# Kernel tuning notes

Hardware: AMD Instinct MI355X
Metric: run time of the kernel (lower is better)

The kernel has to match this reference:

```python
import jax, jax.numpy as jnp
import numpy as np
import math

B, S, D = 2, 2048, 1024
H, KV, HD = 16, 4, 64
N_REP = H // KV
ROPE_THETA = 1.0e6


def _rope_tables(seq_len, head_dim, theta):
    inv_freq = 1.0 / (theta ** (np.arange(0, head_dim, 2, dtype=np.float32) / head_dim))
    t = np.arange(seq_len, dtype=np.float32)
    freqs = np.outer(t, inv_freq)                      # [S, HD/2]
    emb = np.concatenate([freqs, freqs], axis=-1)      # [S, HD]
    return jnp.asarray(np.cos(emb)), jnp.asarray(np.sin(emb))


def setup_inputs() -> dict:
    key = jax.random.key(0)
    ks = jax.random.split(key, 6)
    cos, sin = _rope_tables(S, HD, ROPE_THETA)
    scale = 0.02
    return {
        "x": jax.random.normal(ks[0], (B, S, D), dtype=jnp.float32),
        "cos": cos,
        "sin": sin,
        "Wq": jax.random.normal(ks[1], (D, H * HD), dtype=jnp.float32) * scale,
        "Wk": jax.random.normal(ks[2], (D, KV * HD), dtype=jnp.float32) * scale,
        "Wv": jax.random.normal(ks[3], (D, KV * HD), dtype=jnp.float32) * scale,
        "Wo": jax.random.normal(ks[4], (H * HD, D), dtype=jnp.float32) * scale,
    }


def _rotate_half(u):
    u1, u2 = u[..., : HD // 2], u[..., HD // 2 :]
    return jnp.concatenate([-u2, u1], axis=-1)


def reference(x, cos, sin, Wq, Wk, Wv, Wo):
    bsz, seq_len, _ = x.shape
    q = (x @ Wq).reshape(bsz, seq_len, H, HD)   # [B,S,H,HD]
    k = (x @ Wk).reshape(bsz, seq_len, KV, HD)  # [B,S,KV,HD]
    v = (x @ Wv).reshape(bsz, seq_len, KV, HD)

    # RoPE: cos/sin [S,HD] broadcast over batch and heads (unsqueeze_dim=1)
    c = cos[:seq_len][None, :, None, :]
    s = sin[:seq_len][None, :, None, :]
    q = q * c + _rotate_half(q) * s
    k = k * c + _rotate_half(k) * s

    # repeat_kv: expand KV heads groupwise to H heads
    k = jnp.repeat(k, N_REP, axis=2)  # [B,S,H,HD]
    v = jnp.repeat(v, N_REP, axis=2)

    q = q.transpose(0, 2, 1, 3)  # [B,H,S,HD]
    k = k.transpose(0, 2, 1, 3)
    v = v.transpose(0, 2, 1, 3)

    scores = jnp.einsum("bhqd,bhkd->bhqk", q, k) / math.sqrt(HD)
    causal = jnp.tril(jnp.ones((seq_len, seq_len), dtype=bool))
    scores = jnp.where(causal[None, None], scores, jnp.finfo(jnp.float32).min)
    probs = jax.nn.softmax(scores.astype(jnp.float32), axis=-1).astype(x.dtype)

    out = jnp.einsum("bhqk,bhkd->bhqd", probs, v)        # [B,H,S,HD]
    out = out.transpose(0, 2, 1, 3).reshape(bsz, seq_len, H * HD)
    return out @ Wo
```

## Files before the change

### kernel.cpp

```cpp
#include <hip/hip_runtime.h>

#define SS 2048
#define NH 16
#define NKV 4
#define HD 64

typedef __bf16 bf16;
typedef __bf16 bf16x4 __attribute__((ext_vector_type(4)));
typedef __bf16 bf16x8 __attribute__((ext_vector_type(8)));
typedef float f32x4 __attribute__((ext_vector_type(4)));

#define SM_SCALE 0.18033688011f

__device__ __forceinline__ void gl_lds16(const bf16* g, bf16* l) {
    __builtin_amdgcn_global_load_lds((const __attribute__((address_space(1))) void*)g,
                                     (__attribute__((address_space(3))) void*)l, 16, 0, 0);
}

__global__ __launch_bounds__(256) void prep_kernel(
    const float* __restrict__ x,
    const float* __restrict__ Wq, const float* __restrict__ Wk,
    const float* __restrict__ Wv, const float* __restrict__ Wo,
    bf16* __restrict__ wqkv_t, bf16* __restrict__ wo_t, bf16* __restrict__ xb)
{
    const int blk = blockIdx.x;
    const int tid = threadIdx.x;
    if (blk >= 640) {
        const size_t i0 = (size_t)(blk - 640) * 16384;
        #pragma unroll
        for (int i = 0; i < 16; ++i) {
            const size_t idx = i0 + i * 1024 + tid * 4;
            const float4 v = *(const float4*)&x[idx];
            bf16x4 o4;
            o4[0] = (bf16)v.x; o4[1] = (bf16)v.y; o4[2] = (bf16)v.z; o4[3] = (bf16)v.w;
            *(bf16x4*)&xb[idx] = o4;
        }
        return;
    }
    const float* W; bf16* Wt; int N, n0, k0;
    if (blk < 256)      { W = Wq; Wt = wqkv_t;                       N = 1024; n0 = (blk & 15) * 64;         k0 = (blk >> 4) * 64; }
    else if (blk < 320) { W = Wk; Wt = wqkv_t + (size_t)1024 * 1024; N = 256;  n0 = ((blk - 256) & 3) * 64;  k0 = ((blk - 256) >> 2) * 64; }
    else if (blk < 384) { W = Wv; Wt = wqkv_t + (size_t)1280 * 1024; N = 256;  n0 = ((blk - 320) & 3) * 64;  k0 = ((blk - 320) >> 2) * 64; }
    else                { W = Wo; Wt = wo_t;                         N = 1024; n0 = ((blk - 384) & 15) * 64; k0 = ((blk - 384) >> 4) * 64; }

    __shared__ float Ts[64][65];
    const int c = tid & 63, rr = tid >> 6;
    #pragma unroll
    for (int i = 0; i < 16; ++i) {
        const int kk = i * 4 + rr;
        Ts[kk][c] = W[(size_t)(k0 + kk) * N + n0 + c];
    }
    __syncthreads();
    #pragma unroll
    for (int i = 0; i < 16; ++i) {
        const int nn = i * 4 + rr;
        Wt[(size_t)(n0 + nn) * 1024 + k0 + c] = (bf16)Ts[c][nn];
    }
}

template<int EPI>
__global__ __launch_bounds__(256) void gemm_bt_kernel(
    const bf16* __restrict__ A, const bf16* __restrict__ Bt, float* __restrict__ C,
    const float* __restrict__ cosp, const float* __restrict__ sinp,
    bf16* __restrict__ qo, bf16* __restrict__ ko, bf16* __restrict__ vto,
    int N, int K, int CB)
{
    __shared__ bf16 As[2][64 * 64];
    __shared__ bf16 Bs[2][128 * 64];
    const int bid = blockIdx.x;
    const int j = bid >> 3;
    const int rb = (bid & 7) + 8 * (j / CB);
    const int cb = j % CB;
    const int m0 = rb * 64, n0 = cb * 128;
    const int tid = threadIdx.x;
    const int w = tid >> 6, lane = tid & 63, g = lane >> 4, li = lane & 15;
    const int wm = w >> 1, wn = w & 1;

    f32x4 acc[2][4];
    const f32x4 z = {0.f, 0.f, 0.f, 0.f};
    #pragma unroll
    for (int i = 0; i < 2; ++i)
        #pragma unroll
        for (int jj = 0; jj < 4; ++jj) acc[i][jj] = z;

    const int srow = tid >> 3;
    const int schunk = ((tid & 7) ^ (srow & 7)) * 8;
    const bf16* pA[2];
    const bf16* pB[4];
    #pragma unroll
    for (int s = 0; s < 2; ++s) pA[s] = A + (size_t)(m0 + s * 32 + srow) * K + schunk;
    #pragma unroll
    for (int s = 0; s < 4; ++s) pB[s] = Bt + (size_t)(n0 + s * 32 + srow) * K + schunk;
    const int lw = w * 512;

    const int NT = K >> 6;

    #pragma unroll
    for (int s = 0; s < 2; ++s) gl_lds16(pA[s], &As[0][s * 2048 + lw]);
    #pragma unroll
    for (int s = 0; s < 4; ++s) gl_lds16(pB[s], &Bs[0][s * 2048 + lw]);
    #pragma unroll
    for (int s = 0; s < 2; ++s) gl_lds16(pA[s] + 64, &As[1][s * 2048 + lw]);
    #pragma unroll
    for (int s = 0; s < 4; ++s) gl_lds16(pB[s] + 64, &Bs[1][s * 2048 + lw]);

    for (int t = 0; t < NT; ++t) {
        const int cur = t & 1;
        if (t + 1 < NT) { asm volatile("s_waitcnt vmcnt(6)" ::: "memory"); }
        else            { asm volatile("s_waitcnt vmcnt(0)" ::: "memory"); }
        __builtin_amdgcn_s_barrier();
        #pragma unroll
        for (int tt = 0; tt < 2; ++tt) {
            const int phys = ((tt * 4 + g) ^ (li & 7)) * 8;
            bf16x8 af[2], bfr[4];
            #pragma unroll
            for (int mi = 0; mi < 2; ++mi) af[mi] = *(const bf16x8*)&As[cur][(wm * 32 + mi * 16 + li) * 64 + phys];
            #pragma unroll
            for (int ni = 0; ni < 4; ++ni) bfr[ni] = *(const bf16x8*)&Bs[cur][(wn * 64 + ni * 16 + li) * 64 + phys];
            __builtin_amdgcn_s_setprio(1);
            #pragma unroll
            for (int mi = 0; mi < 2; ++mi)
                #pragma unroll
                for (int ni = 0; ni < 4; ++ni)
                    acc[mi][ni] = __builtin_amdgcn_mfma_f32_16x16x32_bf16(af[mi], bfr[ni], acc[mi][ni], 0, 0, 0);
            __builtin_amdgcn_s_setprio(0);
        }
        __builtin_amdgcn_s_barrier();
        if (t + 2 < NT) {
            const int kk = (t + 2) << 6;
            #pragma unroll
            for (int s = 0; s < 2; ++s) gl_lds16(pA[s] + kk, &As[cur][s * 2048 + lw]);
            #pragma unroll
            for (int s = 0; s < 4; ++s) gl_lds16(pB[s] + kk, &Bs[cur][s * 2048 + lw]);
        }
    }

    const int row0 = m0 + wm * 32, col0 = n0 + wn * 64;
    if (EPI == 0) {
        #pragma unroll
        for (int mi = 0; mi < 2; ++mi)
            #pragma unroll
            for (int ni = 0; ni < 4; ++ni)
                #pragma unroll
                for (int r = 0; r < 4; ++r)
                    C[(size_t)(row0 + mi * 16 + g * 4 + r) * N + col0 + ni * 16 + li] = acc[mi][ni][r];
    } else {
        #pragma unroll
        for (int ni = 0; ni < 4; ++ni) {
            const int col = col0 + ni * 16 + li;
            const int d = col & 63;
            #pragma unroll
            for (int mi = 0; mi < 2; ++mi) {
                #pragma unroll
                for (int r = 0; r < 4; ++r) {
                    const int row = row0 + mi * 16 + g * 4 + r;
                    const int bb = row >> 11, s = row & 2047;
                    float val = acc[mi][ni][r];
                    if (col < 1280) {
                        const float pairv = acc[mi][ni ^ 2][r];
                        const float rot = (d < 32) ? -pairv : pairv;
                        val = val * cosp[s * 64 + d] + rot * sinp[s * 64 + d];
                    }
                    if (col < 1024) {
                        const int hh = col >> 6;
                        qo[(((size_t)bb * NH + hh) * SS + s) * HD + d] = (bf16)(val * SM_SCALE);
                    } else if (col < 1280) {
                        const int kh = (col - 1024) >> 6;
                        ko[(((size_t)bb * NKV + kh) * SS + s) * HD + d] = (bf16)val;
                    } else {
                        const int kh = (col - 1280) >> 6;
                        vto[(((size_t)bb * NKV + kh) * HD + d) * SS + s] = (bf16)val;
                    }
                }
            }
        }
    }
}

__global__ __launch_bounds__(256) void flash_kernel(const bf16* __restrict__ q, const bf16* __restrict__ k,
                                                    const bf16* __restrict__ vt, bf16* __restrict__ o)
{
    __shared__ bf16 Ks[2][64 * 64];
    __shared__ bf16 Vt[2][64 * 64];
    __shared__ bf16 Ps[4][16 * 64];

    const int blk = blockIdx.x;
    const int qt = 31 - (blk >> 5);
    const int h = blk & 15;
    const int b = (blk >> 4) & 1;
    const int kvh = h >> 2;
    const int tid = threadIdx.x;
    const int w = tid >> 6, lane = tid & 63, g = lane >> 4, li = lane & 15;

    const bf16* qh = q + ((size_t)b * NH + h) * SS * HD;
    const bf16* kh = k + ((size_t)b * NKV + kvh) * SS * HD;
    const bf16* vh = vt + ((size_t)b * NKV + kvh) * (size_t)HD * SS;

    bf16x8 ones;
    #pragma unroll
    for (int jj = 0; jj < 8; ++jj) ones[jj] = (bf16)1.0f;
    const f32x4 z = {0.f, 0.f, 0.f, 0.f};

    const bf16* qrow = qh + (size_t)(qt * 64 + w * 16 + li) * HD;
    bf16x8 qf[2];
    qf[0] = *(const bf16x8*)(qrow + g * 8);
    qf[1] = *(const bf16x8*)(qrow + 32 + g * 8);

    const int srow = tid >> 3;
    const int schunk = ((tid & 7) ^ (srow & 7)) * 8;
    const int lw = w * 512;

    const int xm = (li & 7) << 1;

    f32x4 o_acc[4], l_acc;
    #pragma unroll
    for (int nt = 0; nt < 4; ++nt) o_acc[nt] = z;
    l_acc = z;

    #pragma unroll
    for (int s = 0; s < 2; ++s)
        gl_lds16(kh + (size_t)(s * 32 + srow) * HD + schunk, &Ks[0][s * 2048 + lw]);
    #pragma unroll
    for (int s = 0; s < 2; ++s)
        gl_lds16(vh + (size_t)(s * 32 + srow) * SS + schunk, &Vt[0][s * 2048 + lw]);
    if (qt >= 1) {
        #pragma unroll
        for (int s = 0; s < 2; ++s)
            gl_lds16(kh + (size_t)(64 + s * 32 + srow) * HD + schunk, &Ks[1][s * 2048 + lw]);
        #pragma unroll
        for (int s = 0; s < 2; ++s)
            gl_lds16(vh + (size_t)(s * 32 + srow) * SS + 64 + schunk, &Vt[1][s * 2048 + lw]);
    }

    for (int kt = 0; kt <= qt; ++kt) {
        const int cur = kt & 1;
        if (kt < qt) { asm volatile("s_waitcnt vmcnt(4)" ::: "memory"); }
        else         { asm volatile("s_waitcnt vmcnt(0)" ::: "memory"); }
        __builtin_amdgcn_s_barrier();

        f32x4 s_acc[4];
        #pragma unroll
        for (int nt = 0; nt < 4; ++nt) s_acc[nt] = z;
        __builtin_amdgcn_s_setprio(1);
        #pragma unroll
        for (int t = 0; t < 2; ++t)
            #pragma unroll
            for (int nt = 0; nt < 4; ++nt) {
                const bf16x8 kf = *(const bf16x8*)&Ks[cur][(nt * 16 + li) * 64 + (((t * 4 + g) ^ (li & 7)) * 8)];
                s_acc[nt] = __builtin_amdgcn_mfma_f32_16x16x32_bf16(kf, qf[t], s_acc[nt], 0, 0, 0);
            }
        __builtin_amdgcn_s_setprio(0);

        if (kt == qt) {
            const int qrow_in = w * 16 + li;
            #pragma unroll
            for (int nt = 0; nt < 4; ++nt) {
                bf16x4 p4;
                #pragma unroll
                for (int r = 0; r < 4; ++r) {
                    float sv = s_acc[nt][r];
                    if (nt * 16 + g * 4 + r > qrow_in) sv = -1e30f;
                    p4[r] = (bf16)exp2f(sv);
                }
                *(bf16x4*)&Ps[w][li * 64 + (((nt * 4 + g) ^ xm) * 4)] = p4;
            }
        } else {
            #pragma unroll
            for (int nt = 0; nt < 4; ++nt) {
                bf16x4 p4;
                #pragma unroll
                for (int r = 0; r < 4; ++r) p4[r] = (bf16)exp2f(s_acc[nt][r]);
                *(bf16x4*)&Ps[w][li * 64 + (((nt * 4 + g) ^ xm) * 4)] = p4;
            }
        }

        __builtin_amdgcn_s_setprio(1);
        #pragma unroll
        for (int t = 0; t < 2; ++t) {
            const bf16x8 pf = *(const bf16x8*)&Ps[w][li * 64 + (((t * 8 + g * 2) ^ xm) * 4)];
            l_acc = __builtin_amdgcn_mfma_f32_16x16x32_bf16(pf, ones, l_acc, 0, 0, 0);
            #pragma unroll
            for (int nt = 0; nt < 4; ++nt) {
                const bf16x8 vf = *(const bf16x8*)&Vt[cur][(nt * 16 + li) * 64 + (((t * 4 + g) ^ (li & 7)) * 8)];
                o_acc[nt] = __builtin_amdgcn_mfma_f32_16x16x32_bf16(pf, vf, o_acc[nt], 0, 0, 0);
            }
        }
        __builtin_amdgcn_s_setprio(0);

        __builtin_amdgcn_s_barrier();
        if (kt + 2 <= qt) {
            const size_t kq = (size_t)(kt + 2) * 64;
            #pragma unroll
            for (int s = 0; s < 2; ++s)
                gl_lds16(kh + (kq + s * 32 + srow) * HD + schunk, &Ks[cur][s * 2048 + lw]);
            #pragma unroll
            for (int s = 0; s < 2; ++s)
                gl_lds16(vh + (size_t)(s * 32 + srow) * SS + kq + schunk, &Vt[cur][s * 2048 + lw]);
        }
    }

    #pragma unroll
    for (int r = 0; r < 4; ++r) {
        const float inv = 1.f / l_acc[r];
        const int s = qt * 64 + w * 16 + g * 4 + r;
        bf16* orow = o + (((size_t)b * SS + s) * NH + h) * HD;
        #pragma unroll
        for (int nt = 0; nt < 4; ++nt) orow[nt * 16 + li] = (bf16)(o_acc[nt][r] * inv);
    }
}

extern "C" void kernel_launch(void* const* d_in, const int* in_sizes, int n_in,
                              void* d_out, int out_size, void* d_ws, size_t ws_size,
                              hipStream_t stream) {
    const float* x     = (const float*)d_in[0];
    const float* cos_t = (const float*)d_in[1];
    const float* sin_t = (const float*)d_in[2];
    const float* Wq    = (const float*)d_in[3];
    const float* Wk    = (const float*)d_in[4];
    const float* Wv    = (const float*)d_in[5];
    const float* Wo    = (const float*)d_in[6];
    float* out = (float*)d_out;

    char* wsb = (char*)d_ws;
    bf16* o_b    = (bf16*)(wsb);
    bf16* wqkv_t = (bf16*)(wsb + 8388608);
    bf16* wo_t   = (bf16*)(wsb + 11534336);
    bf16* q_b    = (bf16*)(wsb + 13631488);
    bf16* k_b    = (bf16*)(wsb + 22020096);
    bf16* vt_b   = (bf16*)(wsb + 24117248);
    bf16* x_b    = (bf16*)(wsb + 26214400);

    prep_kernel<<<896, 256, 0, stream>>>(x, Wq, Wk, Wv, Wo, wqkv_t, wo_t, x_b);

    gemm_bt_kernel<2><<<768, 256, 0, stream>>>(x_b, wqkv_t, nullptr, cos_t, sin_t,
                                               q_b, k_b, vt_b, 1536, 1024, 12);
    flash_kernel<<<1024, 256, 0, stream>>>(q_b, k_b, vt_b, o_b);
    gemm_bt_kernel<0><<<512, 256, 0, stream>>>(o_b, wo_t, out, nullptr, nullptr,
                                               nullptr, nullptr, nullptr, 1024, 1024, 8);
}
```

Before: 161.8 us.

## Use 128-row query tiles with 8 waves sharing K/V loads in flash kernel

The flash attention kernel now processes 128 query rows per block with 512 threads (8 waves) instead of 64 rows with 256 threads. Each loaded K/V tile is reused by twice as many waves, which halves global-to-LDS traffic per query row. Block scheduling is also reordered so the first 256 blocks take the longest-running tiles in descending order and the rest run in ascending order, to balance causal work. In exchange, waves whose rows lie entirely above the diagonal sit idle at barriers on the last tiles, and there are half as many blocks.

```diff
diff --git a/kernel.cpp b/kernel.cpp
--- a/kernel.cpp
+++ b/kernel.cpp
@@ -177,17 +177,19 @@
     }
 }
 
-__global__ __launch_bounds__(256) void flash_kernel(const bf16* __restrict__ q, const bf16* __restrict__ k,
+__global__ __launch_bounds__(512) void flash_kernel(const bf16* __restrict__ q, const bf16* __restrict__ k,
                                                     const bf16* __restrict__ vt, bf16* __restrict__ o)
 {
     __shared__ bf16 Ks[2][64 * 64];
     __shared__ bf16 Vt[2][64 * 64];
-    __shared__ bf16 Ps[4][16 * 64];
+    __shared__ bf16 Ps[8][16 * 64];
 
     const int blk = blockIdx.x;
-    const int qt = 31 - (blk >> 5);
-    const int h = blk & 15;
-    const int b = (blk >> 4) & 1;
+    int qt, bh;
+    if (blk < 256) { qt = 15 - (blk >> 5);  bh = blk & 31; }
+    else           { qt = (blk - 256) >> 5; bh = (blk - 256) & 31; }
+    const int h = bh & 15;
+    const int b = bh >> 4;
     const int kvh = h >> 2;
     const int tid = threadIdx.x;
     const int w = tid >> 6, lane = tid & 63, g = lane >> 4, li = lane & 15;
@@ -201,7 +203,8 @@
     for (int jj = 0; jj < 8; ++jj) ones[jj] = (bf16)1.0f;
     const f32x4 z = {0.f, 0.f, 0.f, 0.f};
 
-    const bf16* qrow = qh + (size_t)(qt * 64 + w * 16 + li) * HD;
+    const int wrow0 = qt * 128 + w * 16;
+    const bf16* qrow = qh + (size_t)(wrow0 + li) * HD;
     bf16x8 qf[2];
     qf[0] = *(const bf16x8*)(qrow + g * 8);
     qf[1] = *(const bf16x8*)(qrow + 32 + g * 8);
@@ -212,97 +215,88 @@
 
     const int xm = (li & 7) << 1;
 
+    const int nkt = 2 * qt + 2;
+
     f32x4 o_acc[4], l_acc;
     #pragma unroll
     for (int nt = 0; nt < 4; ++nt) o_acc[nt] = z;
     l_acc = z;
 
-    #pragma unroll
-    for (int s = 0; s < 2; ++s)
-        gl_lds16(kh + (size_t)(s * 32 + srow) * HD + schunk, &Ks[0][s * 2048 + lw]);
-    #pragma unroll
-    for (int s = 0; s < 2; ++s)
-        gl_lds16(vh + (size_t)(s * 32 + srow) * SS + schunk, &Vt[0][s * 2048 + lw]);
-    if (qt >= 1) {
-        #pragma unroll
-        for (int s = 0; s < 2; ++s)
-            gl_lds16(kh + (size_t)(64 + s * 32 + srow) * HD + schunk, &Ks[1][s * 2048 + lw]);
-        #pragma unroll
-        for (int s = 0; s < 2; ++s)
-            gl_lds16(vh + (size_t)(s * 32 + srow) * SS + 64 + schunk, &Vt[1][s * 2048 + lw]);
-    }
-
-    for (int kt = 0; kt <= qt; ++kt) {
+    gl_lds16(kh + (size_t)srow * HD + schunk, &Ks[0][lw]);
+    gl_lds16(vh + (size_t)srow * SS + schunk, &Vt[0][lw]);
+    gl_lds16(kh + (size_t)(64 + srow) * HD + schunk, &Ks[1][lw]);
+    gl_lds16(vh + (size_t)srow * SS + 64 + schunk, &Vt[1][lw]);
+
+    for (int kt = 0; kt < nkt; ++kt) {
         const int cur = kt & 1;
-        if (kt < qt) { asm volatile("s_waitcnt vmcnt(4)" ::: "memory"); }
-        else         { asm volatile("s_waitcnt vmcnt(0)" ::: "memory"); }
+        if (kt + 1 < nkt) { asm volatile("s_waitcnt vmcnt(2)" ::: "memory"); }
+        else              { asm volatile("s_waitcnt vmcnt(0)" ::: "memory"); }
         __builtin_amdgcn_s_barrier();
 
-        f32x4 s_acc[4];
-        #pragma unroll
-        for (int nt = 0; nt < 4; ++nt) s_acc[nt] = z;
-        __builtin_amdgcn_s_setprio(1);
-        #pragma unroll
-        for (int t = 0; t < 2; ++t)
-            #pragma unroll
-            for (int nt = 0; nt < 4; ++nt) {
-                const bf16x8 kf = *(const bf16x8*)&Ks[cur][(nt * 16 + li) * 64 + (((t * 4 + g) ^ (li & 7)) * 8)];
-                s_acc[nt] = __builtin_amdgcn_mfma_f32_16x16x32_bf16(kf, qf[t], s_acc[nt], 0, 0, 0);
+        if (kt * 64 <= wrow0 + 15) {
+            f32x4 s_acc[4];
+            #pragma unroll
+            for (int nt = 0; nt < 4; ++nt) s_acc[nt] = z;
+            __builtin_amdgcn_s_setprio(1);
+            #pragma unroll
+            for (int t = 0; t < 2; ++t)
+                #pragma unroll
+                for (int nt = 0; nt < 4; ++nt) {
+                    const bf16x8 kf = *(const bf16x8*)&Ks[cur][(nt * 16 + li) * 64 + (((t * 4 + g) ^ (li & 7)) * 8)];
+                    s_acc[nt] = __builtin_amdgcn_mfma_f32_16x16x32_bf16(kf, qf[t], s_acc[nt], 0, 0, 0);
+                }
+            __builtin_amdgcn_s_setprio(0);
+
+            if (kt >= 2 * qt) {
+                const int qr = wrow0 + li;
+                const int kbase = kt * 64;
+                #pragma unroll
+                for (int nt = 0; nt < 4; ++nt) {
+                    bf16x4 p4;
+                    #pragma unroll
+                    for (int r = 0; r < 4; ++r) {
+                        float sv = s_acc[nt][r];
+                        if (kbase + nt * 16 + g * 4 + r > qr) sv = -1e30f;
+                        p4[r] = (bf16)exp2f(sv);
+                    }
+                    *(bf16x4*)&Ps[w][li * 64 + (((nt * 4 + g) ^ xm) * 4)] = p4;
+                }
+            } else {
+                #pragma unroll
+                for (int nt = 0; nt < 4; ++nt) {
+                    bf16x4 p4;
+                    #pragma unroll
+                    for (int r = 0; r < 4; ++r) p4[r] = (bf16)exp2f(s_acc[nt][r]);
+                    *(bf16x4*)&Ps[w][li * 64 + (((nt * 4 + g) ^ xm) * 4)] = p4;
+                }
             }
-        __builtin_amdgcn_s_setprio(0);
-
-        if (kt == qt) {
-            const int qrow_in = w * 16 + li;
-            #pragma unroll
-            for (int nt = 0; nt < 4; ++nt) {
-                bf16x4 p4;
-                #pragma unroll
-                for (int r = 0; r < 4; ++r) {
-                    float sv = s_acc[nt][r];
-                    if (nt * 16 + g * 4 + r > qrow_in) sv = -1e30f;
-                    p4[r] = (bf16)exp2f(sv);
-                }
-                *(bf16x4*)&Ps[w][li * 64 + (((nt * 4 + g) ^ xm) * 4)] = p4;
+
+            __builtin_amdgcn_s_setprio(1);
+            #pragma unroll
+            for (int t = 0; t < 2; ++t) {
+                const bf16x8 pf = *(const bf16x8*)&Ps[w][li * 64 + (((t * 8 + g * 2) ^ xm) * 4)];
+                l_acc = __builtin_amdgcn_mfma_f32_16x16x32_bf16(pf, ones, l_acc, 0, 0, 0);
+                #pragma unroll
+                for (int nt = 0; nt < 4; ++nt) {
+                    const bf16x8 vf = *(const bf16x8*)&Vt[cur][(nt * 16 + li) * 64 + (((t * 4 + g) ^ (li & 7)) * 8)];
+                    o_acc[nt] = __builtin_amdgcn_mfma_f32_16x16x32_bf16(pf, vf, o_acc[nt], 0, 0, 0);
+                }
             }
-        } else {
-            #pragma unroll
-            for (int nt = 0; nt < 4; ++nt) {
-                bf16x4 p4;
-                #pragma unroll
-                for (int r = 0; r < 4; ++r) p4[r] = (bf16)exp2f(s_acc[nt][r]);
-                *(bf16x4*)&Ps[w][li * 64 + (((nt * 4 + g) ^ xm) * 4)] = p4;
-            }
-        }
-
-        __builtin_amdgcn_s_setprio(1);
-        #pragma unroll
-        for (int t = 0; t < 2; ++t) {
-            const bf16x8 pf = *(const bf16x8*)&Ps[w][li * 64 + (((t * 8 + g * 2) ^ xm) * 4)];
-            l_acc = __builtin_amdgcn_mfma_f32_16x16x32_bf16(pf, ones, l_acc, 0, 0, 0);
-            #pragma unroll
-            for (int nt = 0; nt < 4; ++nt) {
-                const bf16x8 vf = *(const bf16x8*)&Vt[cur][(nt * 16 + li) * 64 + (((t * 4 + g) ^ (li & 7)) * 8)];
-                o_acc[nt] = __builtin_amdgcn_mfma_f32_16x16x32_bf16(pf, vf, o_acc[nt], 0, 0, 0);
-            }
-        }
-        __builtin_amdgcn_s_setprio(0);
+            __builtin_amdgcn_s_setprio(0);
+        }
 
         __builtin_amdgcn_s_barrier();
-        if (kt + 2 <= qt) {
+        if (kt + 2 < nkt) {
             const size_t kq = (size_t)(kt + 2) * 64;
-            #pragma unroll
-            for (int s = 0; s < 2; ++s)
-                gl_lds16(kh + (kq + s * 32 + srow) * HD + schunk, &Ks[cur][s * 2048 + lw]);
-            #pragma unroll
-            for (int s = 0; s < 2; ++s)
-                gl_lds16(vh + (size_t)(s * 32 + srow) * SS + kq + schunk, &Vt[cur][s * 2048 + lw]);
+            gl_lds16(kh + (kq + srow) * HD + schunk, &Ks[cur][lw]);
+            gl_lds16(vh + (size_t)srow * SS + kq + schunk, &Vt[cur][lw]);
         }
     }
 
     #pragma unroll
     for (int r = 0; r < 4; ++r) {
         const float inv = 1.f / l_acc[r];
-        const int s = qt * 64 + w * 16 + g * 4 + r;
+        const int s = wrow0 + g * 4 + r;
         bf16* orow = o + (((size_t)b * SS + s) * NH + h) * HD;
         #pragma unroll
         for (int nt = 0; nt < 4; ++nt) orow[nt * 16 + li] = (bf16)(o_acc[nt][r] * inv);
@@ -334,7 +328,7 @@
 
     gemm_bt_kernel<2><<<768, 256, 0, stream>>>(x_b, wqkv_t, nullptr, cos_t, sin_t,
                                                q_b, k_b, vt_b, 1536, 1024, 12);
-    flash_kernel<<<1024, 256, 0, stream>>>(q_b, k_b, vt_b, o_b);
+    flash_kernel<<<512, 512, 0, stream>>>(q_b, k_b, vt_b, o_b);
     gemm_bt_kernel<0><<<512, 256, 0, stream>>>(o_b, wo_t, out, nullptr, nullptr,
                                                nullptr, nullptr, nullptr, 1024, 1024, 8);
 }
```

New measurement: 169.1 us. 1.05x slower.
